# Performance work log

Measured on AMD Instinct MI355X. Metric: run time of the kernel, lower is better.

## Reference

```python
import jax, jax.numpy as jnp
import numpy as np

ALPHA = 0.2  # LeakyReLU negative slope
NEG_INF = -9e15


def setup_inputs() -> dict:
    key = jax.random.key(0)
    ks = jax.random.split(key, 6)
    N, IN, OUT, E = 2048, 256, 256, 64
    inp = {
        "input": jax.random.normal(ks[0], (N, IN), dtype=jnp.float32),
        "adj": jax.random.randint(ks[1], (N, N), 0, 2, dtype=jnp.int32),
        "e_feat": jax.random.normal(ks[2], (N, N, E), dtype=jnp.float32),
        # xavier-uniform-like scale for params
        "W_e": jax.random.normal(ks[3], (E, IN), dtype=jnp.float32) * (1.414 * np.sqrt(2.0 / (E + IN))),
        "W": jax.random.normal(ks[4], (IN, OUT), dtype=jnp.float32) * (1.414 * np.sqrt(2.0 / (IN + OUT))),
        "a": jax.random.normal(ks[5], (3 * OUT, 1), dtype=jnp.float32) * (1.414 * np.sqrt(2.0 / (3 * OUT + 1))),
    }
    return inp


def reference(input, adj, e_feat, W_e, W, a):
    F = W.shape[1]
    # Decompose attention vector: cat([h_i, h_j, e_ij]) @ a == h_i@a1 + h_j@a2 + e_ij@a3
    a1, a2, a3 = a[:F, 0], a[F:2 * F, 0], a[2 * F:, 0]
    h = input @ W                              # [N, F]
    s_src = h @ a1                             # [N]
    s_dst = h @ a2                             # [N]
    # e_ij @ a3 where e = e_feat @ W_e @ W, folded by associativity into one [N,N] result
    s_edge = e_feat @ (W_e @ (W @ a3))         # [N, N]
    scores = jax.nn.leaky_relu(s_src[:, None] + s_dst[None, :] + s_edge, negative_slope=ALPHA)
    att = jnp.where(adj > 0, scores, NEG_INF)
    att = jax.nn.softmax(att, axis=1)
    h_prime = att @ h                          # [N, F]
    return jax.nn.elu(h_prime)                 # concat=True -> ELU
```

## Files before the change

### kernel.cpp

```cpp
#include <hip/hip_runtime.h>
#include <math.h>

#define NN   2048
#define INF_ 256
#define OUTF 256
#define EF   64
#define ALPHA 0.2f
#define NEG_INF -9000000000000000.0f

typedef unsigned short ushortT;
typedef __attribute__((ext_vector_type(8))) short    short8v;
typedef __attribute__((ext_vector_type(4))) short    short4v;
typedef __attribute__((ext_vector_type(8))) unsigned short u16x8;
typedef __attribute__((ext_vector_type(4))) float    f32x4;

__device__ __forceinline__ float b2f(ushortT u) {
    unsigned v = (unsigned)u << 16;
    return *(float*)&v;
}
__device__ __forceinline__ ushortT f2b(float f) {
    unsigned b = *(unsigned*)&f;
    unsigned r = (b + 0x7FFFu + ((b >> 16) & 1u)) >> 16;
    return (ushortT)r;
}

__global__ void prep1_kernel(const float* __restrict__ W, const float* __restrict__ a,
                             float* __restrict__ w3) {
    int lane = threadIdx.x & 63, wave = threadIdx.x >> 6;
    const float* a3 = a + 2 * OUTF;
    float4 av = *(const float4*)&a3[lane * 4];
    int r0 = blockIdx.x * 8 + wave * 2;
    #pragma unroll
    for (int rr = 0; rr < 2; ++rr) {
        int r = r0 + rr;
        float4 wv = *(const float4*)&W[(size_t)r * OUTF + lane * 4];
        float d = wv.x * av.x + wv.y * av.y + wv.z * av.z + wv.w * av.w;
        #pragma unroll
        for (int off = 32; off; off >>= 1) d += __shfl_xor(d, off);
        if (lane == 0) w3[r] = d;
    }
}

__global__ void prep2_kernel(const float* __restrict__ W_e, const float* __restrict__ w3,
                             float* __restrict__ we3) {
    int lane = threadIdx.x & 63, wave = threadIdx.x >> 6;
    int r = blockIdx.x * 4 + wave;
    float4 wv = *(const float4*)&W_e[(size_t)r * INF_ + lane * 4];
    float4 xv = *(const float4*)&w3[lane * 4];
    float d = wv.x * xv.x + wv.y * xv.y + wv.z * xv.z + wv.w * xv.w;
    #pragma unroll
    for (int off = 32; off; off >>= 1) d += __shfl_xor(d, off);
    if (lane == 0) we3[r] = d;
}

__global__ void sv_kernel(const float* __restrict__ h, const float* __restrict__ a,
                          float* __restrict__ s_src, float* __restrict__ s_dst) {
    int lane = threadIdx.x & 63;
    int wave = threadIdx.x >> 6;
    int i = blockIdx.x * 4 + wave;
    float acc1 = 0.f, acc2 = 0.f;
    #pragma unroll
    for (int u = 0; u < 4; ++u) {
        int o = lane + u * 64;
        float hv = h[(size_t)i * OUTF + o];
        acc1 += hv * a[o];
        acc2 += hv * a[OUTF + o];
    }
    #pragma unroll
    for (int off = 32; off; off >>= 1) {
        acc1 += __shfl_xor(acc1, off);
        acc2 += __shfl_xor(acc2, off);
    }
    if (lane == 0) { s_src[i] = acc1; s_dst[i] = acc2; }
}

template<int K>
__launch_bounds__(256, 2)
__global__ void gemm_kernel(const float* __restrict__ A, const float* __restrict__ Bm,
                            float* __restrict__ C) {
    __shared__ float As[64][68];
    __shared__ float Bs[64][32];
    int tid = threadIdx.x;
    int r0 = blockIdx.x * 64;
    int c0 = blockIdx.y * 32;
    int tr = tid >> 4;
    int tc = tid & 15;
    float acc[4][2] = {};

    for (int k0 = 0; k0 < K; k0 += 64) {
        #pragma unroll
        for (int t = 0; t < 4; ++t) {
            int s = tid + t * 256;
            int row = s >> 4, col4 = s & 15;
            *(float4*)&As[row][col4 * 4] =
                *(const float4*)&A[(size_t)(r0 + row) * K + k0 + col4 * 4];
        }
        #pragma unroll
        for (int t = 0; t < 2; ++t) {
            int s = tid + t * 256;
            int row = s >> 3, col4 = s & 7;
            *(float4*)&Bs[row][col4 * 4] =
                *(const float4*)&Bm[(size_t)(k0 + row) * 256 + c0 + col4 * 4];
        }
        __syncthreads();
        #pragma unroll
        for (int kk = 0; kk < 64; kk += 4) {
            float4 aReg[4];
            float2 bReg[4];
            #pragma unroll
            for (int i = 0; i < 4; ++i) aReg[i] = *(const float4*)&As[tr * 4 + i][kk];
            #pragma unroll
            for (int q = 0; q < 4; ++q)  bReg[q] = *(const float2*)&Bs[kk + q][tc * 2];
            #pragma unroll
            for (int q = 0; q < 4; ++q) {
                float bx = bReg[q].x, by = bReg[q].y;
                #pragma unroll
                for (int i = 0; i < 4; ++i) {
                    float av = (q == 0) ? aReg[i].x : (q == 1) ? aReg[i].y
                             : (q == 2) ? aReg[i].z : aReg[i].w;
                    acc[i][0] += av * bx;
                    acc[i][1] += av * by;
                }
            }
        }
        __syncthreads();
    }
    #pragma unroll
    for (int i = 0; i < 4; ++i) {
        int r = r0 + tr * 4 + i;
        float2 v = {acc[i][0], acc[i][1]};
        *(float2*)&C[(size_t)r * 256 + c0 + tc * 2] = v;
    }
}

__global__ void xpose_kernel(const float* __restrict__ h, ushortT* __restrict__ hbT) {
    __shared__ ushortT tb[64][72];
    int t = threadIdx.x;
    int r0 = blockIdx.x * 64;
    int n0 = blockIdx.y * 64;
    int row = t >> 2, seg = t & 3;
    #pragma unroll
    for (int c = 0; c < 4; ++c) {
        float4 v = *(const float4*)&h[(size_t)(r0 + row) * OUTF + n0 + seg * 16 + c * 4];
        tb[seg * 16 + c * 4 + 0][row] = f2b(v.x);
        tb[seg * 16 + c * 4 + 1][row] = f2b(v.y);
        tb[seg * 16 + c * 4 + 2][row] = f2b(v.z);
        tb[seg * 16 + c * 4 + 3][row] = f2b(v.w);
    }
    __syncthreads();
    *(u16x8*)&hbT[(size_t)(n0 + row) * NN + r0 + seg * 16] =
        *(const u16x8*)&tb[row][seg * 16];
    *(u16x8*)&hbT[(size_t)(n0 + row) * NN + r0 + seg * 16 + 8] =
        *(const u16x8*)&tb[row][seg * 16 + 8];
}

__launch_bounds__(256, 2)
__global__ void gemm2_mfma_kernel(const ushortT* __restrict__ attb,
                                  const ushortT* __restrict__ hbT,
                                  float* __restrict__ Cpart) {
    __shared__ ushortT As[64][72];
    __shared__ ushortT Bs[64][72];
    int tid = threadIdx.x;
    int lane = tid & 63;
    int w = tid >> 6;
    int r0 = blockIdx.x * 64;
    int c0 = blockIdx.y * 64;
    int z  = blockIdx.z;
    int m = lane & 15, q = lane >> 4;
    const int srow = tid >> 2, sseg = tid & 3;

    f32x4 acc0 = {0.f, 0.f, 0.f, 0.f};
    f32x4 acc1 = {0.f, 0.f, 0.f, 0.f};
    f32x4 acc2 = {0.f, 0.f, 0.f, 0.f};
    f32x4 acc3 = {0.f, 0.f, 0.f, 0.f};

    for (int k0 = z * (NN / 4); k0 < (z + 1) * (NN / 4); k0 += 64) {
        {
            const size_t abase = (size_t)(r0 + srow) * NN + k0 + sseg * 16;
            *(u16x8*)&As[srow][sseg * 16]     = *(const u16x8*)&attb[abase];
            *(u16x8*)&As[srow][sseg * 16 + 8] = *(const u16x8*)&attb[abase + 8];
            const size_t bbase = (size_t)(c0 + srow) * NN + k0 + sseg * 16;
            *(u16x8*)&Bs[srow][sseg * 16]     = *(const u16x8*)&hbT[bbase];
            *(u16x8*)&Bs[srow][sseg * 16 + 8] = *(const u16x8*)&hbT[bbase + 8];
        }
        __syncthreads();
        #pragma unroll
        for (int kk = 0; kk < 2; ++kk) {
            short4v a0 = *(const short4v*)&As[w * 16 + m][kk * 32 + q * 4];
            short4v a1 = *(const short4v*)&As[w * 16 + m][kk * 32 + 16 + q * 4];
            short8v af = {a0.x, a0.y, a0.z, a0.w, a1.x, a1.y, a1.z, a1.w};
            #pragma unroll
            for (int nb = 0; nb < 4; ++nb) {
                short4v b0 = *(const short4v*)&Bs[nb * 16 + m][kk * 32 + q * 4];
                short4v b1 = *(const short4v*)&Bs[nb * 16 + m][kk * 32 + 16 + q * 4];
                short8v bf = {b0.x, b0.y, b0.z, b0.w, b1.x, b1.y, b1.z, b1.w};
                if (nb == 0) acc0 = __builtin_amdgcn_mfma_f32_16x16x32_bf16(af, bf, acc0, 0, 0, 0);
                if (nb == 1) acc1 = __builtin_amdgcn_mfma_f32_16x16x32_bf16(af, bf, acc1, 0, 0, 0);
                if (nb == 2) acc2 = __builtin_amdgcn_mfma_f32_16x16x32_bf16(af, bf, acc2, 0, 0, 0);
                if (nb == 3) acc3 = __builtin_amdgcn_mfma_f32_16x16x32_bf16(af, bf, acc3, 0, 0, 0);
            }
        }
        __syncthreads();
    }
    float* Cz = Cpart + (size_t)z * NN * OUTF;
    #pragma unroll
    for (int r = 0; r < 4; ++r) {
        int row = r0 + w * 16 + q * 4 + r;
        Cz[(size_t)row * OUTF + c0 + 0  + m] = acc0[r];
        Cz[(size_t)row * OUTF + c0 + 16 + m] = acc1[r];
        Cz[(size_t)row * OUTF + c0 + 32 + m] = acc2[r];
        Cz[(size_t)row * OUTF + c0 + 48 + m] = acc3[r];
    }
}

__global__ void combine_kernel(const float* __restrict__ Cpart, const float* __restrict__ invs,
                               float* __restrict__ out) {
    int i = blockIdx.x, t = threadIdx.x;
    size_t idx = (size_t)i * OUTF + t;
    const size_t P = (size_t)NN * OUTF;
    float v = (Cpart[idx] + Cpart[P + idx] + Cpart[2 * P + idx] + Cpart[3 * P + idx]) * invs[i];
    out[idx] = v > 0.f ? v : __expf(v) - 1.f;
}

__launch_bounds__(256, 8)
__global__ void score_kernel(const float* __restrict__ e_feat, const int* __restrict__ adj,
                             const float* __restrict__ s_src, const float* __restrict__ s_dst,
                             const float* __restrict__ we3,
                             ushortT* __restrict__ attb, float* __restrict__ invs) {
    __shared__ float p[NN];
    __shared__ float sdst[NN];
    __shared__ unsigned char amask[NN];
    __shared__ float swe3[EF];
    __shared__ float redm[4], reds[4];

    int tid  = threadIdx.x;
    int lane = tid & 63;
    int wave = tid >> 6;
    int i    = blockIdx.x;

    const int* arow = adj + (size_t)i * NN;
    #pragma unroll
    for (int t = 0; t < 2; ++t) {
        int s = tid * 2 + t;
        int4 a4 = ((const int4*)arow)[s];
        uchar4 m4;
        m4.x = a4.x != 0; m4.y = a4.y != 0; m4.z = a4.z != 0; m4.w = a4.w != 0;
        *(uchar4*)&amask[s * 4] = m4;
        ((float4*)sdst)[s] = ((const float4*)s_dst)[s];
    }
    if (tid < EF) swe3[tid] = we3[tid];
    __syncthreads();

    const int g  = lane >> 4;
    const int gl = lane & 15;
    const float4 wv = *(const float4*)&swe3[gl * 4];
    const float ssrc = s_src[i];
    const float* efrow = e_feat + (size_t)i * NN * EF;

    for (int j0 = 0; j0 < NN; j0 += 64) {
        int    av[4];
        float4 ev[4];
        #pragma unroll
        for (int u = 0; u < 4; ++u) {
            int j = j0 + u * 16 + g * 4 + wave;
            av[u] = amask[j];
            if (av[u] != 0)
                ev[u] = *(const float4*)&efrow[(size_t)j * EF + gl * 4];
        }
        #pragma unroll
        for (int u = 0; u < 4; ++u) {
            int j = j0 + u * 16 + g * 4 + wave;
            float sc = NEG_INF;
            if (av[u] != 0) {
                float d = ev[u].x * wv.x + ev[u].y * wv.y + ev[u].z * wv.z + ev[u].w * wv.w;
                d += __shfl_xor(d, 1);
                d += __shfl_xor(d, 2);
                d += __shfl_xor(d, 4);
                d += __shfl_xor(d, 8);
                float s = ssrc + sdst[j] + d;
                sc = (s > 0.f) ? s : ALPHA * s;
            }
            if (gl == 0) p[j] = sc;
        }
    }
    __syncthreads();

    float m = NEG_INF;
    for (int j = tid; j < NN; j += 256) m = fmaxf(m, p[j]);
    #pragma unroll
    for (int off = 32; off; off >>= 1) m = fmaxf(m, __shfl_xor(m, off));
    if (lane == 0) redm[wave] = m;
    __syncthreads();
    m = fmaxf(fmaxf(redm[0], redm[1]), fmaxf(redm[2], redm[3]));

    ushortT* arowo = attb + (size_t)i * NN;
    float sum = 0.f;
    for (int j = tid * 2; j < NN; j += 512) {
        float e0 = __expf(p[j]     - m);
        float e1 = __expf(p[j + 1] - m);
        ushort2 uu; uu.x = f2b(e0); uu.y = f2b(e1);
        *(ushort2*)&arowo[j] = uu;
        sum += e0 + e1;
    }
    #pragma unroll
    for (int off = 32; off; off >>= 1) sum += __shfl_xor(sum, off);
    if (lane == 0) reds[wave] = sum;
    __syncthreads();
    if (tid == 0) invs[i] = 1.f / (reds[0] + reds[1] + reds[2] + reds[3]);
}

extern "C" void kernel_launch(void* const* d_in, const int* in_sizes, int n_in,
                              void* d_out, int out_size, void* d_ws, size_t ws_size,
                              hipStream_t stream) {
    const float* input  = (const float*)d_in[0];
    const int*   adj    = (const int*)  d_in[1];
    const float* e_feat = (const float*)d_in[2];
    const float* W_e    = (const float*)d_in[3];
    const float* W      = (const float*)d_in[4];
    const float* a      = (const float*)d_in[5];
    float* out = (float*)d_out;

    float*   ws    = (float*)d_ws;
    float*   h     = ws;
    float*   s_src = h + (size_t)NN * OUTF;
    float*   s_dst = s_src + NN;
    float*   w3    = s_dst + NN;
    float*   we3   = w3 + INF_;
    float*   invs  = we3 + EF;
    ushortT* attb  = (ushortT*)(invs + NN);
    ushortT* hbT   = attb + (size_t)NN * NN;
    float*   cpart = (float*)(hbT + (size_t)OUTF * NN);

    prep1_kernel<<<32, 256, 0, stream>>>(W, a, w3);
    prep2_kernel<<<16, 256, 0, stream>>>(W_e, w3, we3);
    gemm_kernel<INF_><<<dim3(NN / 64, 8), 256, 0, stream>>>(input, W, h);
    xpose_kernel<<<dim3(NN / 64, OUTF / 64), 256, 0, stream>>>(h, hbT);
    sv_kernel<<<NN / 4, 256, 0, stream>>>(h, a, s_src, s_dst);
    score_kernel<<<NN, 256, 0, stream>>>(e_feat, adj, s_src, s_dst, we3, attb, invs);
    gemm2_mfma_kernel<<<dim3(NN / 64, OUTF / 64, 4), 256, 0, stream>>>(attb, hbT, cpart);
    combine_kernel<<<NN, 256, 0, stream>>>(cpart, invs, out);
}
```

Baseline: 168.6 us.

## Use 4 lanes per edge row with DPP reduction in score kernel

Remaps the score kernel so each edge row of 64 floats is handled by 4 lanes loading four float4s each, instead of 16 lanes loading one float4. The cross-lane sum then needs only two DPP quad-permute adds rather than four shuffles, which cuts shuffle and LDS traffic per edge. Launch bounds are lowered to 6 waves-per-EU occupancy and the loop is unrolled by 2 to allow more loads in flight. Each lane's loads are now strided by row rather than fully contiguous across the wave, which may change how memory accesses coalesce, and occupancy is lower.

```diff
diff --git a/kernel.cpp b/kernel.cpp
--- a/kernel.cpp
+++ b/kernel.cpp
@@ -22,6 +22,18 @@
     unsigned b = *(unsigned*)&f;
     unsigned r = (b + 0x7FFFu + ((b >> 16) & 1u)) >> 16;
     return (ushortT)r;
+}
+__device__ __forceinline__ float dpp_add_xor1(float x) {
+    int xi = *(int*)&x;
+    int r = __builtin_amdgcn_mov_dpp(xi, 0xB1, 0xF, 0xF, true);
+    float rf = *(float*)&r;
+    return x + rf;
+}
+__device__ __forceinline__ float dpp_add_xor2(float x) {
+    int xi = *(int*)&x;
+    int r = __builtin_amdgcn_mov_dpp(xi, 0x4E, 0xF, 0xF, true);
+    float rf = *(float*)&r;
+    return x + rf;
 }
 
 __global__ void prep1_kernel(const float* __restrict__ W, const float* __restrict__ a,
@@ -222,7 +234,7 @@
     out[idx] = v > 0.f ? v : __expf(v) - 1.f;
 }
 
-__launch_bounds__(256, 8)
+__launch_bounds__(256, 6)
 __global__ void score_kernel(const float* __restrict__ e_feat, const int* __restrict__ adj,
                              const float* __restrict__ s_src, const float* __restrict__ s_dst,
                              const float* __restrict__ we3,
@@ -251,37 +263,39 @@
     if (tid < EF) swe3[tid] = we3[tid];
     __syncthreads();
 
-    const int g  = lane >> 4;
-    const int gl = lane & 15;
-    const float4 wv = *(const float4*)&swe3[gl * 4];
+    const int g  = lane >> 2;
+    const int gl = lane & 3;
+    const float4 wv0 = *(const float4*)&swe3[0  + gl * 4];
+    const float4 wv1 = *(const float4*)&swe3[16 + gl * 4];
+    const float4 wv2 = *(const float4*)&swe3[32 + gl * 4];
+    const float4 wv3 = *(const float4*)&swe3[48 + gl * 4];
     const float ssrc = s_src[i];
     const float* efrow = e_feat + (size_t)i * NN * EF;
 
+    #pragma unroll 2
     for (int j0 = 0; j0 < NN; j0 += 64) {
-        int    av[4];
-        float4 ev[4];
-        #pragma unroll
-        for (int u = 0; u < 4; ++u) {
-            int j = j0 + u * 16 + g * 4 + wave;
-            av[u] = amask[j];
-            if (av[u] != 0)
-                ev[u] = *(const float4*)&efrow[(size_t)j * EF + gl * 4];
-        }
-        #pragma unroll
-        for (int u = 0; u < 4; ++u) {
-            int j = j0 + u * 16 + g * 4 + wave;
-            float sc = NEG_INF;
-            if (av[u] != 0) {
-                float d = ev[u].x * wv.x + ev[u].y * wv.y + ev[u].z * wv.z + ev[u].w * wv.w;
-                d += __shfl_xor(d, 1);
-                d += __shfl_xor(d, 2);
-                d += __shfl_xor(d, 4);
-                d += __shfl_xor(d, 8);
-                float s = ssrc + sdst[j] + d;
-                sc = (s > 0.f) ? s : ALPHA * s;
-            }
-            if (gl == 0) p[j] = sc;
-        }
+        int j = j0 + wave * 16 + g;
+        int av = amask[j];
+        float4 e0, e1, e2, e3;
+        if (av) {
+            const float* ep = efrow + (size_t)j * EF;
+            e0 = *(const float4*)&ep[0  + gl * 4];
+            e1 = *(const float4*)&ep[16 + gl * 4];
+            e2 = *(const float4*)&ep[32 + gl * 4];
+            e3 = *(const float4*)&ep[48 + gl * 4];
+        }
+        float sc = NEG_INF;
+        if (av) {
+            float d = e0.x * wv0.x + e0.y * wv0.y + e0.z * wv0.z + e0.w * wv0.w
+                    + e1.x * wv1.x + e1.y * wv1.y + e1.z * wv1.z + e1.w * wv1.w
+                    + e2.x * wv2.x + e2.y * wv2.y + e2.z * wv2.z + e2.w * wv2.w
+                    + e3.x * wv3.x + e3.y * wv3.y + e3.z * wv3.z + e3.w * wv3.w;
+            d = dpp_add_xor1(d);
+            d = dpp_add_xor2(d);
+            float s = ssrc + sdst[j] + d;
+            sc = (s > 0.f) ? s : ALPHA * s;
+        }
+        if (gl == 0) p[j] = sc;
     }
     __syncthreads();
 
```

Result: faster. 151.9 us (-9.9%).
